# Optimization experiments

Measured on AMD Instinct MI355X. Metric: run time of the kernel, lower is better.

## Reference

```python
import jax, jax.numpy as jnp
import numpy as np

H, W, PART = 16, 16, 4
EPS = 1e-5


def _window_rows(h, part):
    # Static, boundary-clamped window row indices, as in position_aware_max.
    pr = h // part
    half = pr // 2
    idx = []
    for i in range(h):
        u, l = i - half, i + half
        if u < 0:
            u, l = 0, pr
        if l > h:
            u, l = h - pr, h
        idx.append(np.arange(u, l))
    return np.stack(idx)  # [h, pr] (uniform length since pr is even)


def _pam(s6, row_idx, dim):
    # s6: [p, g, hr, wr, hc, wc]; row index r = hr*W + wr, col index s = hc*W + wc.
    if dim == 0:
        # per column block i (hc == i): max over rows hr in window, all wr; keep wc
        sc = jnp.moveaxis(s6, 4, 0)  # [hc, p, g, hr, wr, wc]
        f = lambda sci, idx: jnp.take(sci, idx, axis=2).max(axis=(2, 3))
    else:
        # per row block i (hr == i): max over cols hc in window, all wc; keep wr
        sc = jnp.moveaxis(s6, 2, 0)  # [hr, p, g, wr, hc, wc]
        f = lambda sci, idx: jnp.take(sci, idx, axis=3).max(axis=(3, 4))
    out = jax.vmap(f)(sc, jnp.asarray(row_idx))  # [h, p, g, w]
    p, g = s6.shape[0], s6.shape[1]
    return jnp.transpose(out, (1, 2, 0, 3)).reshape(p, g, -1)  # [p, g, hw]


def _bn(x, gamma, beta, axes):
    # BatchNorm in training mode: biased batch statistics (torch default).
    m = x.mean(axis=axes, keepdims=True)
    v = x.var(axis=axes, keepdims=True)
    return gamma * (x - m) * jax.lax.rsqrt(v + EPS) + beta


def setup_inputs() -> dict:
    key = jax.random.key(0)
    k0, k1, k2 = jax.random.split(key, 3)
    p, g, c = 48, 48, 64
    hw = H * W
    return {
        "prob_fea": jax.random.normal(k0, (p, c, H, W), jnp.float32),
        "gal_fea": jax.random.normal(k1, (g, c, H, W), jnp.float32),
        "bn_gamma": jnp.ones((1,), jnp.float32),
        "bn_beta": jnp.zeros((1,), jnp.float32),
        "fc_w": jnp.full((1, hw), 1.0 / hw, jnp.float32),  # reset_parameters fill
        "fc_b": jax.random.normal(k2, (1,), jnp.float32) * 0.01,
        "lbn_gamma": jnp.ones((1,), jnp.float32),
        "lbn_beta": jnp.zeros((1,), jnp.float32),
    }


def reference(prob_fea, gal_fea, bn_gamma, bn_beta, fc_w, fc_b, lbn_gamma, lbn_beta):
    p, c = prob_fea.shape[0], prob_fea.shape[1]
    g = gal_fea.shape[0]
    hw = H * W
    pf = prob_fea.reshape(p, c, hw)
    gf = gal_fea.reshape(g, c, hw)
    score = jnp.einsum('pcs,gcr->pgrs', pf, gf)  # [p, g, hw, hw]
    s6 = score.reshape(p, g, H, W, H, W)
    row_idx = _window_rows(H, PART)
    s1 = _pam(s6, row_idx, 0)  # [p, g, hw]
    s2 = _pam(s6, row_idx, 1)  # [p, g, hw]
    sc = jnp.concatenate([s1, s2], axis=-1).reshape(-1, 1, hw)  # [2*p*g, 1, hw]
    sc = _bn(sc, bn_gamma, bn_beta, (0, 2)).reshape(-1, hw)
    sc = sc @ fc_w.T + fc_b  # [2*p*g, 1]
    sc = sc.reshape(-1, 2).sum(axis=1, keepdims=True)  # [p*g, 1]
    sc = _bn(sc, lbn_gamma, lbn_beta, (0,))
    return jax.nn.sigmoid(sc).reshape(p, g)
```

## Files before the change

### kernel.cpp

```cpp
#include <hip/hip_runtime.h>

typedef __attribute__((ext_vector_type(8))) short short8;
typedef __attribute__((ext_vector_type(4))) float float4v;

__constant__ int LOW[16] = {0,0,0,1,2,3,4,5,6,7,8,9,10,11,12,12};
__constant__ int HIW[16] = {3,3,3,4,5,6,7,8,9,10,11,12,13,14,15,15};

__device__ __forceinline__ unsigned short f2bf(float f) {
    unsigned int x = __builtin_bit_cast(unsigned int, f);
    x += 0x7FFF + ((x >> 16) & 1);
    return (unsigned short)(x >> 16);
}

struct __align__(16) U16x8 { unsigned short u[8]; };

template <int CTRL>
__device__ __forceinline__ float dppmaxf(float x) {
    int y = __builtin_amdgcn_update_dpp(0, __builtin_bit_cast(int, x),
                                        CTRL, 0xF, 0xF, true);
    return fmaxf(x, __builtin_bit_cast(float, y));
}
__device__ __forceinline__ float rowmax16(float x) {
    x = dppmaxf<0xB1>(x);
    x = dppmaxf<0x4E>(x);
    x = dppmaxf<0x141>(x);
    x = dppmaxf<0x140>(x);
    return x;
}

__global__ __launch_bounds__(256) void pretranspose_kernel(
    const float* __restrict__ prob,
    const float* __restrict__ gal,
    unsigned short* __restrict__ outT)
{
    const int img = blockIdx.x;
    const float* src = (img < 48) ? (prob + img * 16384)
                                  : (gal + (img - 48) * 16384);
    unsigned short* dst = outT + img * 16384;
    const int tid = threadIdx.x;
    const int c0 = (tid & 7) * 8;
    const int s0 = (tid >> 3) * 8;
    unsigned short v[8][8];
#pragma unroll
    for (int i = 0; i < 8; ++i) {
        const float* p = src + (c0 + i) * 256 + s0;
        const float4v f0 = *(const float4v*)(p);
        const float4v f1 = *(const float4v*)(p + 4);
        v[i][0] = f2bf(f0.x); v[i][1] = f2bf(f0.y);
        v[i][2] = f2bf(f0.z); v[i][3] = f2bf(f0.w);
        v[i][4] = f2bf(f1.x); v[i][5] = f2bf(f1.y);
        v[i][6] = f2bf(f1.z); v[i][7] = f2bf(f1.w);
    }
#pragma unroll
    for (int j = 0; j < 8; ++j) {
        U16x8 o;
#pragma unroll
        for (int i = 0; i < 8; ++i) o.u[i] = v[i][j];
        const int srow = s0 + j;
        const int off = srow * 64 + (((c0 >> 3) ^ (srow & 7)) << 3);
        *(U16x8*)(dst + off) = o;
    }
}

__global__ __launch_bounds__(256, 4) void score_pam_kernel(
    const unsigned short* __restrict__ preT,
    const float* __restrict__ fcw,
    float* __restrict__ outDot,
    float* __restrict__ outSum,
    float* __restrict__ outSq)
{
    __shared__ unsigned short bufB[256 * 64];
    __shared__ float fcw_lds[256];
    __shared__ float red[4][4][4];

    const int tid = threadIdx.x;
    const int pair = blockIdx.x;
    const int ip = pair / 48;
    const int ig = pair % 48;
    const unsigned short* pimg = preT + ip * 16384;
    const unsigned short* gimg = preT + (48 + ig) * 16384;

    fcw_lds[tid] = fcw[tid];

    const int lane = tid & 63;
    const int w = tid >> 6;
    const int laneM = lane & 15;
    const int q = lane >> 4;
    const int z = laneM & 7;

    float dot = 0.f, sum = 0.f, sq = 0.f;
    const float msk = (laneM == 0) ? 1.0f : 0.0f;

    int lo[4], hi[4];
#pragma unroll
    for (int j = 0; j < 4; ++j) { lo[j] = LOW[4 * w + j]; hi[j] = HIW[4 * w + j]; }

    for (int pass = 0; pass < 2; ++pass) {
        const unsigned short* Bimg = pass ? gimg : pimg;
        const unsigned short* Aimg = pass ? pimg : gimg;
        if (pass) __syncthreads();
#pragma unroll
        for (int j = 0; j < 8; ++j) {
            const int off = j * 2048 + tid * 8;
            *(U16x8*)(bufB + off) = *(const U16x8*)(Bimg + off);
        }

        short8 a0[4], a1[4];
#pragma unroll
        for (int j = 0; j < 4; ++j) {
            const int srow = (4 * w + j) * 16 + laneM;
            a0[j] = *(const short8*)(Aimg + srow * 64 + ((q ^ z) << 3));
            a1[j] = *(const short8*)(Aimg + srow * 64 + (((q + 4) ^ z) << 3));
        }

        float4v run[4];
#pragma unroll
        for (int j = 0; j < 4; ++j)
            run[j] = (float4v){ -3.0e38f, -3.0e38f, -3.0e38f, -3.0e38f };

        __syncthreads();

        int sl = lo[0] * 16 + laneM;
        short8 b0 = *(const short8*)(bufB + sl * 64 + ((q ^ z) << 3));
        short8 b1 = *(const short8*)(bufB + sl * 64 + (((q + 4) ^ z) << 3));
        for (int ct = lo[0]; ct <= hi[3]; ++ct) {
            const int ctn = (ct < hi[3]) ? ct + 1 : ct;
            const int sln = ctn * 16 + laneM;
            const short8 nb0 = *(const short8*)(bufB + sln * 64 + ((q ^ z) << 3));
            const short8 nb1 = *(const short8*)(bufB + sln * 64 + (((q + 4) ^ z) << 3));
#pragma unroll
            for (int j = 0; j < 4; ++j) {
                if (ct >= lo[j] && ct <= hi[j]) {
                    float4v acc = { 0.f, 0.f, 0.f, 0.f };
                    acc = __builtin_amdgcn_mfma_f32_16x16x32_bf16(a0[j], b0, acc, 0, 0, 0);
                    acc = __builtin_amdgcn_mfma_f32_16x16x32_bf16(a1[j], b1, acc, 0, 0, 0);
                    run[j].x = fmaxf(run[j].x, acc.x);
                    run[j].y = fmaxf(run[j].y, acc.y);
                    run[j].z = fmaxf(run[j].z, acc.z);
                    run[j].w = fmaxf(run[j].w, acc.w);
                }
            }
            b0 = nb0; b1 = nb1;
        }

#pragma unroll
        for (int j = 0; j < 4; ++j) {
            float rx = rowmax16(run[j].x);
            float ry = rowmax16(run[j].y);
            float rz = rowmax16(run[j].z);
            float rw = rowmax16(run[j].w);
            const int rt = 4 * w + j;
            const float4v fw = *(const float4v*)(fcw_lds + rt * 16 + q * 4);
            float t;
            t = msk * rx; dot += t * fw.x; sum += t; sq += t * rx;
            t = msk * ry; dot += t * fw.y; sum += t; sq += t * ry;
            t = msk * rz; dot += t * fw.z; sum += t; sq += t * rz;
            t = msk * rw; dot += t * fw.w; sum += t; sq += t * rw;
        }
    }

    if (laneM == 0) {
        red[w][q][0] = dot; red[w][q][1] = sum; red[w][q][2] = sq;
    }
    __syncthreads();
    if (tid < 3) {
        float s = 0.f;
#pragma unroll
        for (int a = 0; a < 4; ++a)
#pragma unroll
            for (int b = 0; b < 4; ++b) s += red[a][b][tid];
        if (tid == 0) outDot[pair] = s;
        else if (tid == 1) outSum[pair] = s;
        else outSq[pair] = s;
    }
}

__global__ __launch_bounds__(256) void finalize_kernel(
    const float* __restrict__ dDot,
    const float* __restrict__ dSum,
    const float* __restrict__ dSq,
    const float* __restrict__ bng,
    const float* __restrict__ bnb,
    const float* __restrict__ fcw,
    const float* __restrict__ fcb,
    const float* __restrict__ lg,
    const float* __restrict__ lb,
    float* __restrict__ outp)
{
    __shared__ float red[12];
    const int tid = threadIdx.x;
    const int lane = tid & 63;
    const int w = tid >> 6;

    float S = 0.f, Q = 0.f;
    float dv[9];
#pragma unroll
    for (int k = 0; k < 9; ++k) {
        const int i = tid + 256 * k;
        dv[k] = dDot[i];
        S += dSum[i];
        Q += dSq[i];
    }
    float Wj = fcw[tid];
#pragma unroll
    for (int d = 32; d >= 1; d >>= 1) {
        S += __shfl_down(S, d, 64);
        Q += __shfl_down(Q, d, 64);
        Wj += __shfl_down(Wj, d, 64);
    }
    if (lane == 0) { red[w] = S; red[4 + w] = Q; red[8 + w] = Wj; }
    __syncthreads();
    S = red[0] + red[1] + red[2] + red[3];
    Q = red[4] + red[5] + red[6] + red[7];
    const float W = red[8] + red[9] + red[10] + red[11];
    __syncthreads();

    const float N1 = 1179648.0f;
    const float m1 = S / N1;
    const float v1 = Q / N1 - m1 * m1;
    const float inv1 = rsqrtf(v1 + 1e-5f);
    const float g1 = bng[0], b1 = bnb[0], fb = fcb[0];
    const float g2 = lg[0], b2 = lb[0];
    const float cA = g1 * inv1;
    const float cB = 2.f * (b1 * W + fb) - cA * 2.f * m1 * W;

    float Sy = 0.f, Qy = 0.f;
    float yv[9];
#pragma unroll
    for (int k = 0; k < 9; ++k) {
        const float y = cA * dv[k] + cB;
        yv[k] = y;
        Sy += y;
        Qy += y * y;
    }
#pragma unroll
    for (int d = 32; d >= 1; d >>= 1) {
        Sy += __shfl_down(Sy, d, 64);
        Qy += __shfl_down(Qy, d, 64);
    }
    if (lane == 0) { red[w] = Sy; red[4 + w] = Qy; }
    __syncthreads();
    Sy = red[0] + red[1] + red[2] + red[3];
    Qy = red[4] + red[5] + red[6] + red[7];

    const float m2 = Sy / 2304.0f;
    const float v2 = Qy / 2304.0f - m2 * m2;
    const float inv2 = rsqrtf(v2 + 1e-5f);
#pragma unroll
    for (int k = 0; k < 9; ++k) {
        const int i = tid + 256 * k;
        const float z = g2 * (yv[k] - m2) * inv2 + b2;
        outp[i] = 1.0f / (1.0f + __expf(-z));
    }
}

extern "C" void kernel_launch(void* const* d_in, const int* in_sizes, int n_in,
                              void* d_out, int out_size, void* d_ws, size_t ws_size,
                              hipStream_t stream) {
    const float* prob = (const float*)d_in[0];
    const float* gal  = (const float*)d_in[1];
    const float* bng  = (const float*)d_in[2];
    const float* bnb  = (const float*)d_in[3];
    const float* fcw  = (const float*)d_in[4];
    const float* fcb  = (const float*)d_in[5];
    const float* lg   = (const float*)d_in[6];
    const float* lb   = (const float*)d_in[7];

    unsigned short* preT = (unsigned short*)d_ws;
    float* ws = (float*)((char*)d_ws + 96 * 16384 * sizeof(unsigned short));
    float* dDot = ws;
    float* dSum = ws + 2304;
    float* dSq  = ws + 4608;

    hipLaunchKernelGGL(pretranspose_kernel, dim3(96), dim3(256), 0, stream,
                       prob, gal, preT);
    hipLaunchKernelGGL(score_pam_kernel, dim3(48 * 48), dim3(256), 0, stream,
                       preT, fcw, dDot, dSum, dSq);
    hipLaunchKernelGGL(finalize_kernel, dim3(1), dim3(256), 0, stream,
                       dDot, dSum, dSq, bng, bnb, fcw, fcb, lg, lb,
                       (float*)d_out);
}
```

Measured before the change: 102.6 us.

## Read B operand directly from global memory instead of staging in LDS

Removes the LDS staging buffer for the B image and the fcw table. MFMA B fragments are now loaded straight from global memory (L1/L2), and the fc weights are held in registers. This drops two block-wide barriers per pass and the 32 KB LDS allocation, which could raise occupancy. In exchange, each wave issues its own global loads for overlapping B tiles, so there is redundant traffic and higher latency inside the dependent MFMA loop.

```diff
diff --git a/kernel.cpp b/kernel.cpp
--- a/kernel.cpp
+++ b/kernel.cpp
@@ -69,8 +69,6 @@
     float* __restrict__ outSum,
     float* __restrict__ outSq)
 {
-    __shared__ unsigned short bufB[256 * 64];
-    __shared__ float fcw_lds[256];
     __shared__ float red[4][4][4];
 
     const int tid = threadIdx.x;
@@ -80,30 +78,27 @@
     const unsigned short* pimg = preT + ip * 16384;
     const unsigned short* gimg = preT + (48 + ig) * 16384;
 
-    fcw_lds[tid] = fcw[tid];
-
     const int lane = tid & 63;
     const int w = tid >> 6;
     const int laneM = lane & 15;
     const int q = lane >> 4;
     const int z = laneM & 7;
 
+    float4v fw[4];
+#pragma unroll
+    for (int j = 0; j < 4; ++j)
+        fw[j] = *(const float4v*)(fcw + (4 * w + j) * 16 + q * 4);
+
+    int lo[4], hi[4];
+#pragma unroll
+    for (int j = 0; j < 4; ++j) { lo[j] = LOW[4 * w + j]; hi[j] = HIW[4 * w + j]; }
+
     float dot = 0.f, sum = 0.f, sq = 0.f;
     const float msk = (laneM == 0) ? 1.0f : 0.0f;
 
-    int lo[4], hi[4];
-#pragma unroll
-    for (int j = 0; j < 4; ++j) { lo[j] = LOW[4 * w + j]; hi[j] = HIW[4 * w + j]; }
-
     for (int pass = 0; pass < 2; ++pass) {
+        const unsigned short* Aimg = pass ? pimg : gimg;
         const unsigned short* Bimg = pass ? gimg : pimg;
-        const unsigned short* Aimg = pass ? pimg : gimg;
-        if (pass) __syncthreads();
-#pragma unroll
-        for (int j = 0; j < 8; ++j) {
-            const int off = j * 2048 + tid * 8;
-            *(U16x8*)(bufB + off) = *(const U16x8*)(Bimg + off);
-        }
 
         short8 a0[4], a1[4];
 #pragma unroll
@@ -118,16 +113,14 @@
         for (int j = 0; j < 4; ++j)
             run[j] = (float4v){ -3.0e38f, -3.0e38f, -3.0e38f, -3.0e38f };
 
-        __syncthreads();
-
         int sl = lo[0] * 16 + laneM;
-        short8 b0 = *(const short8*)(bufB + sl * 64 + ((q ^ z) << 3));
-        short8 b1 = *(const short8*)(bufB + sl * 64 + (((q + 4) ^ z) << 3));
+        short8 b0 = *(const short8*)(Bimg + sl * 64 + ((q ^ z) << 3));
+        short8 b1 = *(const short8*)(Bimg + sl * 64 + (((q + 4) ^ z) << 3));
         for (int ct = lo[0]; ct <= hi[3]; ++ct) {
             const int ctn = (ct < hi[3]) ? ct + 1 : ct;
             const int sln = ctn * 16 + laneM;
-            const short8 nb0 = *(const short8*)(bufB + sln * 64 + ((q ^ z) << 3));
-            const short8 nb1 = *(const short8*)(bufB + sln * 64 + (((q + 4) ^ z) << 3));
+            const short8 nb0 = *(const short8*)(Bimg + sln * 64 + ((q ^ z) << 3));
+            const short8 nb1 = *(const short8*)(Bimg + sln * 64 + (((q + 4) ^ z) << 3));
 #pragma unroll
             for (int j = 0; j < 4; ++j) {
                 if (ct >= lo[j] && ct <= hi[j]) {
@@ -149,13 +142,11 @@
             float ry = rowmax16(run[j].y);
             float rz = rowmax16(run[j].z);
             float rw = rowmax16(run[j].w);
-            const int rt = 4 * w + j;
-            const float4v fw = *(const float4v*)(fcw_lds + rt * 16 + q * 4);
             float t;
-            t = msk * rx; dot += t * fw.x; sum += t; sq += t * rx;
-            t = msk * ry; dot += t * fw.y; sum += t; sq += t * ry;
-            t = msk * rz; dot += t * fw.z; sum += t; sq += t * rz;
-            t = msk * rw; dot += t * fw.w; sum += t; sq += t * rw;
+            t = msk * rx; dot += t * fw[j].x; sum += t; sq += t * rx;
+            t = msk * ry; dot += t * fw[j].y; sum += t; sq += t * ry;
+            t = msk * rz; dot += t * fw[j].z; sum += t; sq += t * rz;
+            t = msk * rw; dot += t * fw[j].w; sum += t; sq += t * rw;
         }
     }
 
```

Measured after the change: 104.0 us. About the same (+1.4%).

## Compute both pooled maxima from one score pass instead of two transposed passes

Applied to the files above, without the earlier changes.

Each score tile is now computed once, and both the row-window max (s2) and the column-window max (s1) are derived from the same MFMA result. Before, the kernel ran two passes with the probe and gallery roles swapped. s1 partial maxima are reduced across waves through LDS, with a shuffle reduction for the dot, sum and square-sum terms. The LDS staging buffer for B is dropped: B tiles are read directly from global memory per wave, trading shared-memory reuse for fewer MFMAs and less LDS. Each wave now covers 8 column tiles, so some tiles are computed that serve only one of the two maxima.

```diff
diff --git a/kernel.cpp b/kernel.cpp
--- a/kernel.cpp
+++ b/kernel.cpp
@@ -3,8 +3,11 @@
 typedef __attribute__((ext_vector_type(8))) short short8;
 typedef __attribute__((ext_vector_type(4))) float float4v;
 
-__constant__ int LOW[16] = {0,0,0,1,2,3,4,5,6,7,8,9,10,11,12,12};
-__constant__ int HIW[16] = {3,3,3,4,5,6,7,8,9,10,11,12,13,14,15,15};
+__constant__ int LOW[24] = {0,0,0,1,2,3,4,5,6,7,8,9,10,11,12,12,
+                            99,99,99,99,99,99,99,99};
+__constant__ int HIW[24] = {3,3,3,4,5,6,7,8,9,10,11,12,13,14,15,15,
+                            -1,-1,-1,-1,-1,-1,-1,-1};
+__constant__ int CTLO[4] = {0, 2, 6, 10};
 
 __device__ __forceinline__ unsigned short f2bf(float f) {
     unsigned int x = __builtin_bit_cast(unsigned int, f);
@@ -69,9 +72,9 @@
     float* __restrict__ outSum,
     float* __restrict__ outSq)
 {
-    __shared__ unsigned short bufB[256 * 64];
-    __shared__ float fcw_lds[256];
-    __shared__ float red[4][4][4];
+    __shared__ float s1part[4][8][4][16];
+    __shared__ float redA[4][4][4];
+    __shared__ float redB[4][4];
 
     const int tid = threadIdx.x;
     const int pair = blockIdx.x;
@@ -80,95 +83,120 @@
     const unsigned short* pimg = preT + ip * 16384;
     const unsigned short* gimg = preT + (48 + ig) * 16384;
 
-    fcw_lds[tid] = fcw[tid];
-
     const int lane = tid & 63;
     const int w = tid >> 6;
     const int laneM = lane & 15;
     const int q = lane >> 4;
     const int z = laneM & 7;
 
-    float dot = 0.f, sum = 0.f, sq = 0.f;
-    const float msk = (laneM == 0) ? 1.0f : 0.0f;
-
-    int lo[4], hi[4];
-#pragma unroll
-    for (int j = 0; j < 4; ++j) { lo[j] = LOW[4 * w + j]; hi[j] = HIW[4 * w + j]; }
-
-    for (int pass = 0; pass < 2; ++pass) {
-        const unsigned short* Bimg = pass ? gimg : pimg;
-        const unsigned short* Aimg = pass ? pimg : gimg;
-        if (pass) __syncthreads();
-#pragma unroll
-        for (int j = 0; j < 8; ++j) {
-            const int off = j * 2048 + tid * 8;
-            *(U16x8*)(bufB + off) = *(const U16x8*)(Bimg + off);
-        }
-
-        short8 a0[4], a1[4];
+    const int rtb = 4 * w;
+    int lo2[4], hi2[4];
+#pragma unroll
+    for (int j = 0; j < 4; ++j) { lo2[j] = LOW[rtb + j]; hi2[j] = HIW[rtb + j]; }
+    const int ctbase = CTLO[w];
+
+    short8 a0[4], a1[4];
+#pragma unroll
+    for (int j = 0; j < 4; ++j) {
+        const int srow = (rtb + j) * 16 + laneM;
+        a0[j] = *(const short8*)(gimg + srow * 64 + ((q ^ z) << 3));
+        a1[j] = *(const short8*)(gimg + srow * 64 + (((q + 4) ^ z) << 3));
+    }
+
+    float4v run[4];
+#pragma unroll
+    for (int j = 0; j < 4; ++j)
+        run[j] = (float4v){ -3.0e38f, -3.0e38f, -3.0e38f, -3.0e38f };
+    float s1p[8];
+#pragma unroll
+    for (int i = 0; i < 8; ++i) s1p[i] = -3.0e38f;
+
+#pragma unroll
+    for (int i = 0; i < 8; ++i) {
+        const int ctr = ctbase + i;
+        const int ctc = (ctr > 15) ? 15 : ctr;
+        const int sl = ctc * 16 + laneM;
+        const short8 b0 = *(const short8*)(pimg + sl * 64 + ((q ^ z) << 3));
+        const short8 b1 = *(const short8*)(pimg + sl * 64 + (((q + 4) ^ z) << 3));
+        const int wl = LOW[ctr], wh = HIW[ctr];
 #pragma unroll
         for (int j = 0; j < 4; ++j) {
-            const int srow = (4 * w + j) * 16 + laneM;
-            a0[j] = *(const short8*)(Aimg + srow * 64 + ((q ^ z) << 3));
-            a1[j] = *(const short8*)(Aimg + srow * 64 + (((q + 4) ^ z) << 3));
-        }
-
-        float4v run[4];
-#pragma unroll
-        for (int j = 0; j < 4; ++j)
-            run[j] = (float4v){ -3.0e38f, -3.0e38f, -3.0e38f, -3.0e38f };
-
-        __syncthreads();
-
-        int sl = lo[0] * 16 + laneM;
-        short8 b0 = *(const short8*)(bufB + sl * 64 + ((q ^ z) << 3));
-        short8 b1 = *(const short8*)(bufB + sl * 64 + (((q + 4) ^ z) << 3));
-        for (int ct = lo[0]; ct <= hi[3]; ++ct) {
-            const int ctn = (ct < hi[3]) ? ct + 1 : ct;
-            const int sln = ctn * 16 + laneM;
-            const short8 nb0 = *(const short8*)(bufB + sln * 64 + ((q ^ z) << 3));
-            const short8 nb1 = *(const short8*)(bufB + sln * 64 + (((q + 4) ^ z) << 3));
-#pragma unroll
-            for (int j = 0; j < 4; ++j) {
-                if (ct >= lo[j] && ct <= hi[j]) {
-                    float4v acc = { 0.f, 0.f, 0.f, 0.f };
-                    acc = __builtin_amdgcn_mfma_f32_16x16x32_bf16(a0[j], b0, acc, 0, 0, 0);
-                    acc = __builtin_amdgcn_mfma_f32_16x16x32_bf16(a1[j], b1, acc, 0, 0, 0);
+            const int rt = rtb + j;
+            const bool c2 = (ctr >= lo2[j]) && (ctr <= hi2[j]);
+            const bool c1 = (rt >= wl) && (rt <= wh);
+            if (c1 || c2) {
+                float4v acc = { 0.f, 0.f, 0.f, 0.f };
+                acc = __builtin_amdgcn_mfma_f32_16x16x32_bf16(a0[j], b0, acc, 0, 0, 0);
+                acc = __builtin_amdgcn_mfma_f32_16x16x32_bf16(a1[j], b1, acc, 0, 0, 0);
+                if (c2) {
                     run[j].x = fmaxf(run[j].x, acc.x);
                     run[j].y = fmaxf(run[j].y, acc.y);
                     run[j].z = fmaxf(run[j].z, acc.z);
                     run[j].w = fmaxf(run[j].w, acc.w);
                 }
+                if (c1) {
+                    const float t = fmaxf(fmaxf(acc.x, acc.y), fmaxf(acc.z, acc.w));
+                    s1p[i] = fmaxf(s1p[i], t);
+                }
             }
-            b0 = nb0; b1 = nb1;
         }
-
-#pragma unroll
-        for (int j = 0; j < 4; ++j) {
-            float rx = rowmax16(run[j].x);
-            float ry = rowmax16(run[j].y);
-            float rz = rowmax16(run[j].z);
-            float rw = rowmax16(run[j].w);
-            const int rt = 4 * w + j;
-            const float4v fw = *(const float4v*)(fcw_lds + rt * 16 + q * 4);
-            float t;
-            t = msk * rx; dot += t * fw.x; sum += t; sq += t * rx;
-            t = msk * ry; dot += t * fw.y; sum += t; sq += t * ry;
-            t = msk * rz; dot += t * fw.z; sum += t; sq += t * rz;
-            t = msk * rw; dot += t * fw.w; sum += t; sq += t * rw;
+    }
+
+    float dot = 0.f, sum = 0.f, sq = 0.f;
+    const float msk = (laneM == 0) ? 1.0f : 0.0f;
+#pragma unroll
+    for (int j = 0; j < 4; ++j) {
+        const float rx = rowmax16(run[j].x);
+        const float ry = rowmax16(run[j].y);
+        const float rz = rowmax16(run[j].z);
+        const float rw = rowmax16(run[j].w);
+        const float4v fw = *(const float4v*)(fcw + (rtb + j) * 16 + q * 4);
+        float t;
+        t = msk * rx; dot += t * fw.x; sum += t; sq += t * rx;
+        t = msk * ry; dot += t * fw.y; sum += t; sq += t * ry;
+        t = msk * rz; dot += t * fw.z; sum += t; sq += t * rz;
+        t = msk * rw; dot += t * fw.w; sum += t; sq += t * rw;
+    }
+    if (laneM == 0) { redA[w][q][0] = dot; redA[w][q][1] = sum; redA[w][q][2] = sq; }
+
+#pragma unroll
+    for (int i = 0; i < 8; ++i) s1part[w][i][q][laneM] = s1p[i];
+    __syncthreads();
+
+    {
+        const int hc = tid >> 4;
+        const int col = tid & 15;
+        float v = -3.0e38f;
+#pragma unroll
+        for (int wv = 0; wv < 4; ++wv) {
+            const int ii = hc - CTLO[wv];
+            if (ii >= 0 && ii < 8) {
+#pragma unroll
+                for (int q2 = 0; q2 < 4; ++q2)
+                    v = fmaxf(v, s1part[wv][ii][q2][col]);
+            }
         }
-    }
-
-    if (laneM == 0) {
-        red[w][q][0] = dot; red[w][q][1] = sum; red[w][q][2] = sq;
-    }
-    __syncthreads();
+        float d1 = v * fcw[tid];
+        float s1v = v;
+        float q1 = v * v;
+#pragma unroll
+        for (int d = 32; d >= 1; d >>= 1) {
+            d1 += __shfl_down(d1, d, 64);
+            s1v += __shfl_down(s1v, d, 64);
+            q1 += __shfl_down(q1, d, 64);
+        }
+        if (lane == 0) { redB[w][0] = d1; redB[w][1] = s1v; redB[w][2] = q1; }
+    }
+    __syncthreads();
+
     if (tid < 3) {
         float s = 0.f;
 #pragma unroll
-        for (int a = 0; a < 4; ++a)
-#pragma unroll
-            for (int b = 0; b < 4; ++b) s += red[a][b][tid];
+        for (int a = 0; a < 4; ++a) {
+#pragma unroll
+            for (int b = 0; b < 4; ++b) s += redA[a][b][tid];
+            s += redB[a][tid];
+        }
         if (tid == 0) outDot[pair] = s;
         else if (tid == 1) outSum[pair] = s;
         else outSq[pair] = s;
```

After: 97.91 us. 4.6% less time.

## Compute both PAM directions from one score tile pass, one wave per pair

Applied to the files above, without the earlier changes.

The score kernel now gives each wavefront one probe-gallery pair instead of a whole block, and drops the LDS staging and block barriers. It computes each 16x16 score tile once and uses it for both the column-window and row-window max reductions, instead of running two passes over transposed roles. Operands are read straight from global memory and cache, and the final reduction uses DPP and shuffles. The pretranspose kernel is split into quarter-image blocks to spread the work over more blocks. Dropping LDS reuse puts more load traffic on the caches, and the unrolled 16-element running-max array raises register pressure.

```diff
diff --git a/kernel.cpp b/kernel.cpp
--- a/kernel.cpp
+++ b/kernel.cpp
@@ -2,9 +2,6 @@
 
 typedef __attribute__((ext_vector_type(8))) short short8;
 typedef __attribute__((ext_vector_type(4))) float float4v;
-
-__constant__ int LOW[16] = {0,0,0,1,2,3,4,5,6,7,8,9,10,11,12,12};
-__constant__ int HIW[16] = {3,3,3,4,5,6,7,8,9,10,11,12,13,14,15,15};
 
 __device__ __forceinline__ unsigned short f2bf(float f) {
     unsigned int x = __builtin_bit_cast(unsigned int, f);
@@ -19,6 +16,12 @@
     int y = __builtin_amdgcn_update_dpp(0, __builtin_bit_cast(int, x),
                                         CTRL, 0xF, 0xF, true);
     return fmaxf(x, __builtin_bit_cast(float, y));
+}
+template <int CTRL>
+__device__ __forceinline__ float dppaddf(float x) {
+    int y = __builtin_amdgcn_update_dpp(0, __builtin_bit_cast(int, x),
+                                        CTRL, 0xF, 0xF, true);
+    return x + __builtin_bit_cast(float, y);
 }
 __device__ __forceinline__ float rowmax16(float x) {
     x = dppmaxf<0xB1>(x);
@@ -27,19 +30,27 @@
     x = dppmaxf<0x140>(x);
     return x;
 }
-
-__global__ __launch_bounds__(256) void pretranspose_kernel(
+__device__ __forceinline__ float rowsum16(float x) {
+    x = dppaddf<0xB1>(x);
+    x = dppaddf<0x4E>(x);
+    x = dppaddf<0x141>(x);
+    x = dppaddf<0x140>(x);
+    return x;
+}
+
+__global__ __launch_bounds__(64) void pretranspose_kernel(
     const float* __restrict__ prob,
     const float* __restrict__ gal,
     unsigned short* __restrict__ outT)
 {
-    const int img = blockIdx.x;
+    const int img = blockIdx.x >> 2;
+    const int quarter = blockIdx.x & 3;
     const float* src = (img < 48) ? (prob + img * 16384)
                                   : (gal + (img - 48) * 16384);
     unsigned short* dst = outT + img * 16384;
     const int tid = threadIdx.x;
     const int c0 = (tid & 7) * 8;
-    const int s0 = (tid >> 3) * 8;
+    const int s0 = quarter * 64 + (tid >> 3) * 8;
     unsigned short v[8][8];
 #pragma unroll
     for (int i = 0; i < 8; ++i) {
@@ -62,116 +73,98 @@
     }
 }
 
-__global__ __launch_bounds__(256, 4) void score_pam_kernel(
+__global__ __launch_bounds__(256) void score_pam_kernel(
     const unsigned short* __restrict__ preT,
     const float* __restrict__ fcw,
     float* __restrict__ outDot,
     float* __restrict__ outSum,
     float* __restrict__ outSq)
 {
-    __shared__ unsigned short bufB[256 * 64];
-    __shared__ float fcw_lds[256];
-    __shared__ float red[4][4][4];
+    constexpr int cLOW[16] = {0,0,0,1,2,3,4,5,6,7,8,9,10,11,12,12};
+    constexpr int cHIW[16] = {3,3,3,4,5,6,7,8,9,10,11,12,13,14,15,15};
 
     const int tid = threadIdx.x;
-    const int pair = blockIdx.x;
+    const int w = tid >> 6;
+    const int lane = tid & 63;
+    const int pair = blockIdx.x * 4 + w;
     const int ip = pair / 48;
     const int ig = pair % 48;
     const unsigned short* pimg = preT + ip * 16384;
     const unsigned short* gimg = preT + (48 + ig) * 16384;
 
-    fcw_lds[tid] = fcw[tid];
-
-    const int lane = tid & 63;
-    const int w = tid >> 6;
     const int laneM = lane & 15;
     const int q = lane >> 4;
     const int z = laneM & 7;
+    const int ch0 = (q ^ z) << 3;
+    const int ch1 = ((q + 4) ^ z) << 3;
 
     float dot = 0.f, sum = 0.f, sq = 0.f;
     const float msk = (laneM == 0) ? 1.0f : 0.0f;
-
-    int lo[4], hi[4];
-#pragma unroll
-    for (int j = 0; j < 4; ++j) { lo[j] = LOW[4 * w + j]; hi[j] = HIW[4 * w + j]; }
-
-    for (int pass = 0; pass < 2; ++pass) {
-        const unsigned short* Bimg = pass ? gimg : pimg;
-        const unsigned short* Aimg = pass ? pimg : gimg;
-        if (pass) __syncthreads();
-#pragma unroll
-        for (int j = 0; j < 8; ++j) {
-            const int off = j * 2048 + tid * 8;
-            *(U16x8*)(bufB + off) = *(const U16x8*)(Bimg + off);
-        }
-
-        short8 a0[4], a1[4];
-#pragma unroll
-        for (int j = 0; j < 4; ++j) {
-            const int srow = (4 * w + j) * 16 + laneM;
-            a0[j] = *(const short8*)(Aimg + srow * 64 + ((q ^ z) << 3));
-            a1[j] = *(const short8*)(Aimg + srow * 64 + (((q + 4) ^ z) << 3));
-        }
-
-        float4v run[4];
-#pragma unroll
-        for (int j = 0; j < 4; ++j)
-            run[j] = (float4v){ -3.0e38f, -3.0e38f, -3.0e38f, -3.0e38f };
-
-        __syncthreads();
-
-        int sl = lo[0] * 16 + laneM;
-        short8 b0 = *(const short8*)(bufB + sl * 64 + ((q ^ z) << 3));
-        short8 b1 = *(const short8*)(bufB + sl * 64 + (((q + 4) ^ z) << 3));
-        for (int ct = lo[0]; ct <= hi[3]; ++ct) {
-            const int ctn = (ct < hi[3]) ? ct + 1 : ct;
-            const int sln = ctn * 16 + laneM;
-            const short8 nb0 = *(const short8*)(bufB + sln * 64 + ((q ^ z) << 3));
-            const short8 nb1 = *(const short8*)(bufB + sln * 64 + (((q + 4) ^ z) << 3));
-#pragma unroll
-            for (int j = 0; j < 4; ++j) {
-                if (ct >= lo[j] && ct <= hi[j]) {
-                    float4v acc = { 0.f, 0.f, 0.f, 0.f };
-                    acc = __builtin_amdgcn_mfma_f32_16x16x32_bf16(a0[j], b0, acc, 0, 0, 0);
-                    acc = __builtin_amdgcn_mfma_f32_16x16x32_bf16(a1[j], b1, acc, 0, 0, 0);
-                    run[j].x = fmaxf(run[j].x, acc.x);
-                    run[j].y = fmaxf(run[j].y, acc.y);
-                    run[j].z = fmaxf(run[j].z, acc.z);
-                    run[j].w = fmaxf(run[j].w, acc.w);
+    const float msk1 = (q == 0) ? 1.0f : 0.0f;
+
+    float s1p[16];
+#pragma unroll
+    for (int i = 0; i < 16; ++i) s1p[i] = -3.0e38f;
+
+#pragma unroll
+    for (int rt = 0; rt < 16; ++rt) {
+        const int srow = rt * 16 + laneM;
+        const short8 a0 = *(const short8*)(gimg + srow * 64 + ch0);
+        const short8 a1 = *(const short8*)(gimg + srow * 64 + ch1);
+
+        float4v run = { -3.0e38f, -3.0e38f, -3.0e38f, -3.0e38f };
+#pragma unroll
+        for (int ct = 0; ct < 16; ++ct) {
+            const bool c2 = (ct >= cLOW[rt]) && (ct <= cHIW[rt]);
+            const bool c1 = (rt >= cLOW[ct]) && (rt <= cHIW[ct]);
+            if (c1 || c2) {
+                const int sl = ct * 16 + laneM;
+                const short8 b0 = *(const short8*)(pimg + sl * 64 + ch0);
+                const short8 b1 = *(const short8*)(pimg + sl * 64 + ch1);
+                float4v acc = { 0.f, 0.f, 0.f, 0.f };
+                acc = __builtin_amdgcn_mfma_f32_16x16x32_bf16(a0, b0, acc, 0, 0, 0);
+                acc = __builtin_amdgcn_mfma_f32_16x16x32_bf16(a1, b1, acc, 0, 0, 0);
+                if (c2) {
+                    run.x = fmaxf(run.x, acc.x);
+                    run.y = fmaxf(run.y, acc.y);
+                    run.z = fmaxf(run.z, acc.z);
+                    run.w = fmaxf(run.w, acc.w);
+                }
+                if (c1) {
+                    const float t = fmaxf(fmaxf(acc.x, acc.y), fmaxf(acc.z, acc.w));
+                    s1p[ct] = fmaxf(s1p[ct], t);
                 }
             }
-            b0 = nb0; b1 = nb1;
         }
-
-#pragma unroll
-        for (int j = 0; j < 4; ++j) {
-            float rx = rowmax16(run[j].x);
-            float ry = rowmax16(run[j].y);
-            float rz = rowmax16(run[j].z);
-            float rw = rowmax16(run[j].w);
-            const int rt = 4 * w + j;
-            const float4v fw = *(const float4v*)(fcw_lds + rt * 16 + q * 4);
-            float t;
-            t = msk * rx; dot += t * fw.x; sum += t; sq += t * rx;
-            t = msk * ry; dot += t * fw.y; sum += t; sq += t * ry;
-            t = msk * rz; dot += t * fw.z; sum += t; sq += t * rz;
-            t = msk * rw; dot += t * fw.w; sum += t; sq += t * rw;
-        }
-    }
-
-    if (laneM == 0) {
-        red[w][q][0] = dot; red[w][q][1] = sum; red[w][q][2] = sq;
-    }
-    __syncthreads();
-    if (tid < 3) {
-        float s = 0.f;
-#pragma unroll
-        for (int a = 0; a < 4; ++a)
-#pragma unroll
-            for (int b = 0; b < 4; ++b) s += red[a][b][tid];
-        if (tid == 0) outDot[pair] = s;
-        else if (tid == 1) outSum[pair] = s;
-        else outSq[pair] = s;
+        const float rx = rowmax16(run.x);
+        const float ry = rowmax16(run.y);
+        const float rz = rowmax16(run.z);
+        const float rw = rowmax16(run.w);
+        const float4v fw = *(const float4v*)(fcw + rt * 16 + q * 4);
+        float t;
+        t = msk * rx; dot += t * fw.x; sum += t; sq += t * rx;
+        t = msk * ry; dot += t * fw.y; sum += t; sq += t * ry;
+        t = msk * rz; dot += t * fw.z; sum += t; sq += t * rz;
+        t = msk * rw; dot += t * fw.w; sum += t; sq += t * rw;
+    }
+
+#pragma unroll
+    for (int ct = 0; ct < 16; ++ct) {
+        float v = s1p[ct];
+        v = fmaxf(v, __shfl_xor(v, 16, 64));
+        v = fmaxf(v, __shfl_xor(v, 32, 64));
+        const float fv = fcw[ct * 16 + laneM];
+        const float tt = msk1 * v;
+        dot += tt * fv; sum += tt; sq += tt * v;
+    }
+
+    dot = rowsum16(dot); dot += __shfl_xor(dot, 16, 64); dot += __shfl_xor(dot, 32, 64);
+    sum = rowsum16(sum); sum += __shfl_xor(sum, 16, 64); sum += __shfl_xor(sum, 32, 64);
+    sq  = rowsum16(sq);  sq  += __shfl_xor(sq, 16, 64);  sq  += __shfl_xor(sq, 32, 64);
+    if (lane == 0) {
+        outDot[pair] = dot;
+        outSum[pair] = sum;
+        outSq[pair] = sq;
     }
 }
 
@@ -272,9 +265,9 @@
     float* dSum = ws + 2304;
     float* dSq  = ws + 4608;
 
-    hipLaunchKernelGGL(pretranspose_kernel, dim3(96), dim3(256), 0, stream,
+    hipLaunchKernelGGL(pretranspose_kernel, dim3(384), dim3(64), 0, stream,
                        prob, gal, preT);
-    hipLaunchKernelGGL(score_pam_kernel, dim3(48 * 48), dim3(256), 0, stream,
+    hipLaunchKernelGGL(score_pam_kernel, dim3(576), dim3(256), 0, stream,
                        preT, fcw, dDot, dSum, dSq);
     hipLaunchKernelGGL(finalize_kernel, dim3(1), dim3(256), 0, stream,
                        dDot, dSum, dSq, bng, bnb, fcw, fcb, lg, lb,
```

Result: faster. 95.36 us (-7.1%).
